# Performance work log

Measured on AMD Instinct MI355X. Metric: run time of the kernel, lower is better.

## Reference

```python
import jax, jax.numpy as jnp
import numpy as np

B, S, D, H = 4, 2048, 512, 8
DEPTH = D // H
EPS = 1e-6

def setup_inputs() -> dict:
    key = jax.random.key(0)
    ks = jax.random.split(key, 5)
    scale = 1.0 / np.sqrt(D)
    return {
        "x": jax.random.normal(ks[0], (B, S, D), dtype=jnp.float32),
        "wq": jax.random.normal(ks[1], (D, D), dtype=jnp.float32) * scale,
        "wk": jax.random.normal(ks[2], (D, D), dtype=jnp.float32) * scale,
        "wv": jax.random.normal(ks[3], (D, D), dtype=jnp.float32) * scale,
        "wo": jax.random.normal(ks[4], (D, D), dtype=jnp.float32) * scale,
        "bo": jnp.zeros((D,), dtype=jnp.float32),
        "gamma": jnp.ones((D,), dtype=jnp.float32),
        "beta": jnp.zeros((D,), dtype=jnp.float32),
    }

def _split_heads(t):
    # [B,S,D] -> [B,H,S,depth]
    return t.reshape(B, S, H, DEPTH).transpose(0, 2, 1, 3)

def reference(x, wq, wk, wv, wo, bo, gamma, beta):
    q = _split_heads(x @ wq)
    k = _split_heads(x @ wk)
    v = _split_heads(x @ wv)
    logits = jnp.einsum("bhqd,bhkd->bhqk", q, k) / jnp.sqrt(jnp.float32(DEPTH))
    attn = jax.nn.softmax(logits, axis=-1)  # dropout is identity at inference
    ctx = jnp.einsum("bhqk,bhkd->bhqd", attn, v)
    ctx = ctx.transpose(0, 2, 1, 3).reshape(B, S, D)
    out = ctx @ wo + bo
    resid = x + out  # output dropout identity at inference
    mu = jnp.mean(resid, axis=-1, keepdims=True)
    var = jnp.mean(jnp.square(resid - mu), axis=-1, keepdims=True)
    return (resid - mu) / jnp.sqrt(var + EPS) * gamma + beta
```

## Files before the change

### kernel.cpp

```cpp
#include <hip/hip_runtime.h>
#include <hip/hip_bf16.h>

typedef __attribute__((ext_vector_type(8))) short short8;
typedef __attribute__((ext_vector_type(4))) float f32x4;

constexpr int B_ = 4, S_ = 2048, D_ = 512, H_ = 8, DP_ = 64;
constexpr int M_ = B_ * S_;

__device__ __forceinline__ unsigned short f2b(float f) {
    __hip_bfloat16 h = __float2bfloat16(f);
    return *reinterpret_cast<unsigned short*>(&h);
}

__device__ __forceinline__ void gload_lds16(const unsigned short* g, unsigned short* l) {
    __builtin_amdgcn_global_load_lds((const __attribute__((address_space(1))) void*)g,
                                     (__attribute__((address_space(3))) void*)l, 16, 0, 0);
}

#define MFMA16(a, b, c) __builtin_amdgcn_mfma_f32_16x16x32_bf16((a), (b), (c), 0, 0, 0)
#define ASM_BAR() asm volatile("s_barrier" ::: "memory")

__global__ __launch_bounds__(256)
void prep(const float* __restrict__ x, unsigned short* __restrict__ xb,
          const float* __restrict__ w0, const float* __restrict__ w1,
          const float* __restrict__ w2, const float* __restrict__ w3,
          unsigned short* __restrict__ outw) {
    __shared__ float t[64][65];
    int bx = blockIdx.x;
    int tid = threadIdx.x;
    if (bx < 4096) {
        int i = bx * 256 + tid;
        float4 v = ((const float4*)x)[i];
        ushort4 o;
        o.x = f2b(v.x); o.y = f2b(v.y); o.z = f2b(v.z); o.w = f2b(v.w);
        ((ushort4*)xb)[i] = o;
        return;
    }
    int b = bx - 4096;
    int z = b >> 6, r = b & 63;
    int k0 = (r >> 3) * 64, n0 = (r & 7) * 64;
    const float* in = (z == 0) ? w0 : (z == 1) ? w1 : (z == 2) ? w2 : w3;
    unsigned short* out = outw + (size_t)z * D_ * D_;
    int tx = tid & 63, ty = tid >> 6;
#pragma unroll
    for (int i = 0; i < 16; i++) {
        int rr = ty * 16 + i;
        t[rr][tx] = in[(size_t)(k0 + rr) * D_ + n0 + tx];
    }
    __syncthreads();
#pragma unroll
    for (int i = 0; i < 16; i++) {
        int rr = ty * 16 + i;
        out[(size_t)(n0 + rr) * D_ + k0 + tx] = f2b(t[tx][rr]);
    }
}

__global__ __launch_bounds__(256, 2)
void gemm_qkvv(const unsigned short* __restrict__ X,
               const unsigned short* __restrict__ Wt,
               unsigned short* __restrict__ QKV,
               unsigned short* __restrict__ Vt) {
    int z = blockIdx.z;
    int tid = threadIdx.x;
    int wave = tid >> 6, lane = tid & 63, l16 = lane & 15, quad = lane >> 4;
    int wm = (wave >> 1) * 64, wn = (wave & 1) * 64;

    int m0, n0, bb = 0;
    const unsigned short *Abase, *Bbase;
    if (z < 2) {
        m0 = blockIdx.x * 128; n0 = blockIdx.y * 128;
        Abase = X + (size_t)m0 * D_;
        Bbase = Wt + (size_t)z * D_ * D_ + (size_t)n0 * D_;
    } else {
        int idx = blockIdx.y * 64 + blockIdx.x;
        bb = idx >> 6;
        int r = idx & 63;
        m0 = (r & 3) * 128;
        n0 = (r >> 2) * 128;
        Abase = Wt + 2 * (size_t)D_ * D_ + (size_t)m0 * D_;
        Bbase = X + ((size_t)bb * S_ + n0) * D_;
    }

    __shared__ __align__(16) unsigned short SM[32768];
    unsigned short (*Cs)[136] = reinterpret_cast<unsigned short(*)[136]>(SM);

    const int psw = l16 & 7;
    const int drow = lane >> 3;
    const int dsw = (lane & 7) ^ drow;

    auto stage = [&](int t, int b) {
        int k0 = t * 64;
        unsigned short* As = SM + b * 16384;
        unsigned short* Bs = SM + b * 16384 + 8192;
#pragma unroll
        for (int j = 0; j < 4; j++) {
            int r8 = wave * 32 + j * 8;
            gload_lds16(Abase + (size_t)(r8 + drow) * D_ + k0 + dsw * 8, As + r8 * 64);
            gload_lds16(Bbase + (size_t)(r8 + drow) * D_ + k0 + dsw * 8, Bs + r8 * 64);
        }
    };

    f32x4 acc[4][4];
    const f32x4 zf = {0.f, 0.f, 0.f, 0.f};
#pragma unroll
    for (int i = 0; i < 4; i++)
#pragma unroll
        for (int j = 0; j < 4; j++) acc[i][j] = zf;

    stage(0, 0);
    stage(1, 1);
    asm volatile("s_waitcnt vmcnt(8)" ::: "memory");
    ASM_BAR();

    for (int t = 0; t < 8; t++) {
        int b = t & 1;
        const unsigned short* As = SM + b * 16384;
        const unsigned short* Bs = SM + b * 16384 + 8192;
#pragma unroll
        for (int h = 0; h < 2; h++) {
            short8 af[4], bf[4];
#pragma unroll
            for (int mt = 0; mt < 4; mt++)
                af[mt] = *(const short8*)(As + (wm + mt * 16 + l16) * 64 + ((h * 4 + quad) ^ psw) * 8);
#pragma unroll
            for (int nt = 0; nt < 4; nt++)
                bf[nt] = *(const short8*)(Bs + (wn + nt * 16 + l16) * 64 + ((h * 4 + quad) ^ psw) * 8);
#pragma unroll
            for (int nt = 0; nt < 4; nt++)
#pragma unroll
                for (int mt = 0; mt < 4; mt++)
                    acc[nt][mt] = MFMA16(bf[nt], af[mt], acc[nt][mt]);
        }
        if (t < 7) {
            ASM_BAR();
            if (t < 6) {
                stage(t + 2, b);
                asm volatile("s_waitcnt vmcnt(8)" ::: "memory");
            } else {
                asm volatile("s_waitcnt vmcnt(0)" ::: "memory");
            }
            ASM_BAR();
        }
    }
    __syncthreads();
#pragma unroll
    for (int nt = 0; nt < 4; nt++)
#pragma unroll
        for (int mt = 0; mt < 4; mt++) {
            ushort4 pk;
            pk.x = f2b(acc[nt][mt][0]); pk.y = f2b(acc[nt][mt][1]);
            pk.z = f2b(acc[nt][mt][2]); pk.w = f2b(acc[nt][mt][3]);
            *(ushort4*)&Cs[wm + mt * 16 + l16][wn + nt * 16 + quad * 4] = pk;
        }
    __syncthreads();
    if (z < 2) {
        unsigned short* out = QKV + (size_t)z * M_ * D_;
#pragma unroll
        for (int i = 0; i < 8; i++) {
            int c = tid + i * 256;
            int ml = c >> 4, nch = c & 15;
            int m = m0 + ml, n = n0 + nch * 8;
            int b2 = m >> 11, ss = m & 2047, hh = n >> 6, dd = n & 63;
            *(short8*)(out + ((((size_t)b2 * H_ + hh) * S_ + ss) * DP_ + dd)) =
                *(const short8*)&Cs[ml][nch * 8];
        }
    } else {
#pragma unroll
        for (int i = 0; i < 8; i++) {
            int c = tid + i * 256;
            int ml = c >> 4, nch = c & 15;
            *(short8*)(Vt + ((size_t)bb * D_ + m0 + ml) * S_ + n0 + nch * 8) =
                *(const short8*)&Cs[ml][nch * 8];
        }
    }
}

__global__ __launch_bounds__(256, 3)
void flash_attn(const unsigned short* __restrict__ Qg, const unsigned short* __restrict__ Kg,
                const unsigned short* __restrict__ Vt, unsigned short* __restrict__ ctx) {
    int bid0 = blockIdx.x;
    int bid = (bid0 & 7) * 64 + (bid0 >> 3);
    int qt = bid & 15, hh = (bid >> 4) & 7, bb = bid >> 7;
    int tid = threadIdx.x;
    int wave = tid >> 6, lane = tid & 63, l16 = lane & 15, quad = lane >> 4;
    int qh = quad >> 1, ql = quad & 1;

    size_t bh = ((size_t)bb * H_ + hh) * S_ * DP_;
    const unsigned short* Qb = Qg + bh;
    const unsigned short* Kb = Kg + bh;
    const unsigned short* Vb = Vt + bh;

    __shared__ __align__(16) unsigned short Kls[2][64][64];
    __shared__ __align__(16) unsigned short Vls[2][64][64];
    __shared__ __align__(16) unsigned short Ps[4][32][64];

    const int psw = l16 & 7;
    const int drow = (lane >> 3) & 7;
    const int dsw = (lane & 7) ^ drow;

    short8 qa0, qa1, qb0, qb1;
    {
        const unsigned short* qp = Qb + (size_t)(qt * 128 + wave * 32 + l16) * DP_ + quad * 8;
        qa0 = *(const short8*)qp;
        qa1 = *(const short8*)(qp + 32);
        qb0 = *(const short8*)(qp + 16 * DP_);
        qb1 = *(const short8*)(qp + 16 * DP_ + 32);
    }

    auto stage = [&](int kv, int b) {
#pragma unroll
        for (int j = 0; j < 2; j++) {
            int r8 = (wave * 2 + j) * 8;
            int r = r8 + drow;
            gload_lds16(Kb + (size_t)(kv + r) * DP_ + dsw * 8, &Kls[b][r8][0]);
            gload_lds16(Vb + (size_t)r * S_ + kv + dsw * 8,    &Vls[b][r8][0]);
        }
    };

    stage(0, 0);
    stage(64, 1);
    asm volatile("s_waitcnt vmcnt(4)" ::: "memory");
    ASM_BAR();

    const f32x4 zf = {0.f, 0.f, 0.f, 0.f};
    f32x4 oa[4], ob[4];
#pragma unroll
    for (int i = 0; i < 4; i++) { oa[i] = zf; ob[i] = zf; }
    float m2a = -1e30f, m2b = -1e30f;
    float lsa = 0.f, lsb = 0.f;
    constexpr float c1 = 0.125f * 1.44269504088896f;

    int cur = 0;
    for (int t = 0; t < 32; t++) {
        __builtin_amdgcn_s_setprio(1);
        f32x4 sa[4], sb[4];
#pragma unroll
        for (int nt = 0; nt < 4; nt++) {
            const unsigned short* kr = &Kls[cur][nt * 16 + l16][0];
            short8 kf0 = *(const short8*)(kr + ((quad ^ psw) * 8));
            short8 kf1 = *(const short8*)(kr + (((quad ^ 4) ^ psw) * 8));
            f32x4 s = zf;
            s = MFMA16(kf0, qa0, s);
            s = MFMA16(kf1, qa1, s);
            sa[nt] = s;
            s = zf;
            s = MFMA16(kf0, qb0, s);
            s = MFMA16(kf1, qb1, s);
            sb[nt] = s;
        }
        __builtin_amdgcn_s_setprio(0);

        float ga, gb;
        {
            float ta[4], tb[4];
#pragma unroll
            for (int nt = 0; nt < 4; nt++) {
                ta[nt] = fmaxf(fmaxf(sa[nt][0], sa[nt][1]), fmaxf(sa[nt][2], sa[nt][3]));
                tb[nt] = fmaxf(fmaxf(sb[nt][0], sb[nt][1]), fmaxf(sb[nt][2], sb[nt][3]));
            }
            ga = fmaxf(fmaxf(ta[0], ta[1]), fmaxf(ta[2], ta[3]));
            gb = fmaxf(fmaxf(tb[0], tb[1]), fmaxf(tb[2], tb[3]));
        }
        ga = fmaxf(ga, __shfl_xor(ga, 16));
        ga = fmaxf(ga, __shfl_xor(ga, 32));
        gb = fmaxf(gb, __shfl_xor(gb, 16));
        gb = fmaxf(gb, __shfl_xor(gb, 32));
        ga *= c1; gb *= c1;
        float ala = 1.0f, alb = 1.0f;
        bool need = !__all((ga <= m2a + 8.0f) && (gb <= m2b + 8.0f));
        if (need) {
            float na = fmaxf(m2a, ga), nb = fmaxf(m2b, gb);
            ala = __builtin_amdgcn_exp2f(m2a - na);
            alb = __builtin_amdgcn_exp2f(m2b - nb);
            m2a = na; m2b = nb;
        }
        float rsa = 0.f, rsb = 0.f;
#pragma unroll
        for (int nt = 0; nt < 4; nt++) {
            float a0 = __builtin_amdgcn_exp2f(__builtin_fmaf(sa[nt][0], c1, -m2a));
            float a1 = __builtin_amdgcn_exp2f(__builtin_fmaf(sa[nt][1], c1, -m2a));
            float a2 = __builtin_amdgcn_exp2f(__builtin_fmaf(sa[nt][2], c1, -m2a));
            float a3 = __builtin_amdgcn_exp2f(__builtin_fmaf(sa[nt][3], c1, -m2a));
            rsa += (a0 + a1) + (a2 + a3);
            ushort4 pk;
            pk.x = f2b(a0); pk.y = f2b(a1); pk.z = f2b(a2); pk.w = f2b(a3);
            int c8 = (2 * nt + qh) ^ psw;
            *(ushort4*)&Ps[wave][l16][c8 * 8 + 4 * ql] = pk;
            float b0 = __builtin_amdgcn_exp2f(__builtin_fmaf(sb[nt][0], c1, -m2b));
            float b1 = __builtin_amdgcn_exp2f(__builtin_fmaf(sb[nt][1], c1, -m2b));
            float b2 = __builtin_amdgcn_exp2f(__builtin_fmaf(sb[nt][2], c1, -m2b));
            float b3 = __builtin_amdgcn_exp2f(__builtin_fmaf(sb[nt][3], c1, -m2b));
            rsb += (b0 + b1) + (b2 + b3);
            pk.x = f2b(b0); pk.y = f2b(b1); pk.z = f2b(b2); pk.w = f2b(b3);
            *(ushort4*)&Ps[wave][16 + l16][c8 * 8 + 4 * ql] = pk;
        }
        rsa += __shfl_xor(rsa, 16);
        rsa += __shfl_xor(rsa, 32);
        rsb += __shfl_xor(rsb, 16);
        rsb += __shfl_xor(rsb, 32);
        lsa = ala * lsa + rsa;
        lsb = alb * lsb + rsb;
        if (need) {
            float a0 = __shfl(ala, quad * 4 + 0), a1 = __shfl(ala, quad * 4 + 1);
            float a2 = __shfl(ala, quad * 4 + 2), a3 = __shfl(ala, quad * 4 + 3);
            float b0 = __shfl(alb, quad * 4 + 0), b1 = __shfl(alb, quad * 4 + 1);
            float b2 = __shfl(alb, quad * 4 + 2), b3 = __shfl(alb, quad * 4 + 3);
#pragma unroll
            for (int ot = 0; ot < 4; ot++) {
                oa[ot][0] *= a0; oa[ot][1] *= a1; oa[ot][2] *= a2; oa[ot][3] *= a3;
                ob[ot][0] *= b0; ob[ot][1] *= b1; ob[ot][2] *= b2; ob[ot][3] *= b3;
            }
        }

        __builtin_amdgcn_s_setprio(1);
#pragma unroll
        for (int kt = 0; kt < 2; kt++) {
            int pc = ((kt * 4 + quad) ^ psw) * 8;
            short8 pfA = *(const short8*)&Ps[wave][l16][pc];
            short8 pfB = *(const short8*)&Ps[wave][16 + l16][pc];
#pragma unroll
            for (int ot = 0; ot < 4; ot++) {
                short8 vf = *(const short8*)&Vls[cur][ot * 16 + l16][pc];
                oa[ot] = MFMA16(pfA, vf, oa[ot]);
                ob[ot] = MFMA16(pfB, vf, ob[ot]);
            }
        }
        __builtin_amdgcn_s_setprio(0);

        ASM_BAR();
        if (t < 30) {
            stage((t + 2) * 64, cur);
            asm volatile("s_waitcnt vmcnt(4)" ::: "memory");
        } else {
            asm volatile("s_waitcnt vmcnt(0)" ::: "memory");
        }
        ASM_BAR();
        cur ^= 1;
    }

    float la0 = __shfl(lsa, quad * 4 + 0), la1 = __shfl(lsa, quad * 4 + 1);
    float la2 = __shfl(lsa, quad * 4 + 2), la3 = __shfl(lsa, quad * 4 + 3);
    float lb0 = __shfl(lsb, quad * 4 + 0), lb1 = __shfl(lsb, quad * 4 + 1);
    float lb2 = __shfl(lsb, quad * 4 + 2), lb3 = __shfl(lsb, quad * 4 + 3);
    float ia0 = __builtin_amdgcn_rcpf(la0), ia1 = __builtin_amdgcn_rcpf(la1);
    float ia2 = __builtin_amdgcn_rcpf(la2), ia3 = __builtin_amdgcn_rcpf(la3);
    float ib0 = __builtin_amdgcn_rcpf(lb0), ib1 = __builtin_amdgcn_rcpf(lb1);
    float ib2 = __builtin_amdgcn_rcpf(lb2), ib3 = __builtin_amdgcn_rcpf(lb3);
    int srow0 = qt * 128 + wave * 32 + quad * 4;
#pragma unroll
    for (int ot = 0; ot < 4; ot++) {
        size_t base = ((size_t)bb * S_ + srow0) * D_ + hh * DP_ + ot * 16 + l16;
        ctx[base]          = f2b(oa[ot][0] * ia0);
        ctx[base + D_]     = f2b(oa[ot][1] * ia1);
        ctx[base + 2 * D_] = f2b(oa[ot][2] * ia2);
        ctx[base + 3 * D_] = f2b(oa[ot][3] * ia3);
        size_t baseB = base + (size_t)16 * D_;
        ctx[baseB]          = f2b(ob[ot][0] * ib0);
        ctx[baseB + D_]     = f2b(ob[ot][1] * ib1);
        ctx[baseB + 2 * D_] = f2b(ob[ot][2] * ib2);
        ctx[baseB + 3 * D_] = f2b(ob[ot][3] * ib3);
    }
}

__global__ __launch_bounds__(256, 2)
void gemm_proj(const unsigned short* __restrict__ A,
               const unsigned short* __restrict__ Bt,
               float* __restrict__ outf) {
    int m0 = blockIdx.x * 128, n0 = blockIdx.y * 128;
    int tid = threadIdx.x;
    int wave = tid >> 6, lane = tid & 63, l16 = lane & 15, quad = lane >> 4;
    int wm = (wave >> 1) * 64, wn = (wave & 1) * 64;

    __shared__ __align__(16) unsigned short SM[32768];

    const int psw = l16 & 7;
    const int drow = lane >> 3;
    const int dsw = (lane & 7) ^ drow;

    const unsigned short* Abase = A + (size_t)m0 * D_;
    const unsigned short* Bbase = Bt + (size_t)n0 * D_;

    auto stage = [&](int t, int b) {
        int k0 = t * 64;
        unsigned short* As = SM + b * 16384;
        unsigned short* Bs = SM + b * 16384 + 8192;
#pragma unroll
        for (int j = 0; j < 4; j++) {
            int r8 = wave * 32 + j * 8;
            gload_lds16(Abase + (size_t)(r8 + drow) * D_ + k0 + dsw * 8, As + r8 * 64);
            gload_lds16(Bbase + (size_t)(r8 + drow) * D_ + k0 + dsw * 8, Bs + r8 * 64);
        }
    };

    f32x4 acc[4][4];
    const f32x4 zf = {0.f, 0.f, 0.f, 0.f};
#pragma unroll
    for (int i = 0; i < 4; i++)
#pragma unroll
        for (int j = 0; j < 4; j++) acc[i][j] = zf;

    stage(0, 0);
    stage(1, 1);
    asm volatile("s_waitcnt vmcnt(8)" ::: "memory");
    ASM_BAR();

    for (int t = 0; t < 8; t++) {
        int b = t & 1;
        const unsigned short* As = SM + b * 16384;
        const unsigned short* Bs = SM + b * 16384 + 8192;
#pragma unroll
        for (int h = 0; h < 2; h++) {
            short8 af[4], bf[4];
#pragma unroll
            for (int mt = 0; mt < 4; mt++)
                af[mt] = *(const short8*)(As + (wm + mt * 16 + l16) * 64 + ((h * 4 + quad) ^ psw) * 8);
#pragma unroll
            for (int nt = 0; nt < 4; nt++)
                bf[nt] = *(const short8*)(Bs + (wn + nt * 16 + l16) * 64 + ((h * 4 + quad) ^ psw) * 8);
#pragma unroll
            for (int nt = 0; nt < 4; nt++)
#pragma unroll
                for (int mt = 0; mt < 4; mt++)
                    acc[nt][mt] = MFMA16(bf[nt], af[mt], acc[nt][mt]);
        }
        if (t < 7) {
            ASM_BAR();
            if (t < 6) {
                stage(t + 2, b);
                asm volatile("s_waitcnt vmcnt(8)" ::: "memory");
            } else {
                asm volatile("s_waitcnt vmcnt(0)" ::: "memory");
            }
            ASM_BAR();
        }
    }
#pragma unroll
    for (int nt = 0; nt < 4; nt++)
#pragma unroll
        for (int mt = 0; mt < 4; mt++) {
            int m = m0 + wm + mt * 16 + l16;
            int n = n0 + wn + nt * 16 + quad * 4;
            *(f32x4*)&outf[(size_t)m * D_ + n] = acc[nt][mt];
        }
}

__global__ __launch_bounds__(256, 8)
void ln_out(const float* __restrict__ tmp, const float* __restrict__ Xg,
            const float* __restrict__ bo, const float* __restrict__ gamma,
            const float* __restrict__ beta, float* __restrict__ outp) {
    int wave = threadIdx.x >> 6, lane = threadIdx.x & 63;
    int row = blockIdx.x * 4 + wave;
    const float4* t4 = (const float4*)(tmp + (size_t)row * D_);
    const float4* x4 = (const float4*)(Xg + (size_t)row * D_);
    const float4* b4 = (const float4*)bo;
    const float4* g4 = (const float4*)gamma;
    const float4* e4 = (const float4*)beta;
    float4* o4 = (float4*)(outp + (size_t)row * D_);

    float4 r[2];
    float sum = 0.f, sq = 0.f;
#pragma unroll
    for (int i = 0; i < 2; i++) {
        int c = lane + i * 64;
        float4 a = t4[c], x = x4[c], b = b4[c];
        r[i].x = a.x + x.x + b.x;
        r[i].y = a.y + x.y + b.y;
        r[i].z = a.z + x.z + b.z;
        r[i].w = a.w + x.w + b.w;
        sum += (r[i].x + r[i].y) + (r[i].z + r[i].w);
        sq += (r[i].x * r[i].x + r[i].y * r[i].y) + (r[i].z * r[i].z + r[i].w * r[i].w);
    }
#pragma unroll
    for (int off = 1; off < 64; off <<= 1) {
        sum += __shfl_xor(sum, off);
        sq += __shfl_xor(sq, off);
    }
    float mu = sum * (1.0f / D_);
    float var = sq * (1.0f / D_) - mu * mu;
    float rstd = rsqrtf(var + 1e-6f);
#pragma unroll
    for (int i = 0; i < 2; i++) {
        int c = lane + i * 64;
        float4 g = g4[c], e = e4[c];
        float4 o;
        o.x = (r[i].x - mu) * rstd * g.x + e.x;
        o.y = (r[i].y - mu) * rstd * g.y + e.y;
        o.z = (r[i].z - mu) * rstd * g.z + e.z;
        o.w = (r[i].w - mu) * rstd * g.w + e.w;
        o4[c] = o;
    }
}

extern "C" void kernel_launch(void* const* d_in, const int* in_sizes, int n_in,
                              void* d_out, int out_size, void* d_ws, size_t ws_size,
                              hipStream_t stream) {
    const float* x     = (const float*)d_in[0];
    const float* wq    = (const float*)d_in[1];
    const float* wk    = (const float*)d_in[2];
    const float* wv    = (const float*)d_in[3];
    const float* wo    = (const float*)d_in[4];
    const float* bo    = (const float*)d_in[5];
    const float* gamma = (const float*)d_in[6];
    const float* beta  = (const float*)d_in[7];
    float* out = (float*)d_out;

    unsigned short* xb  = (unsigned short*)d_ws;
    unsigned short* wt  = xb + (size_t)M_ * D_;
    unsigned short* Q   = wt + 4 * D_ * D_;
    unsigned short* K   = Q + (size_t)M_ * D_;
    unsigned short* Vt  = K + (size_t)M_ * D_;
    unsigned short* ctx = xb;
    float* tmp = (float*)Q;

    prep<<<dim3(4096 + 256), 256, 0, stream>>>(x, xb, wq, wk, wv, wo, wt);
    gemm_qkvv<<<dim3(64, 4, 3), 256, 0, stream>>>(xb, wt, Q, Vt);
    flash_attn<<<dim3(512), 256, 0, stream>>>(Q, K, Vt, ctx);
    gemm_proj<<<dim3(64, 4), 256, 0, stream>>>(ctx, wt + 3 * (size_t)D_ * D_, tmp);
    ln_out<<<dim3(2048), 256, 0, stream>>>(tmp, x, bo, gamma, beta, out);
}
```

Before: 178.2 us.

## Widen flash-attention KV tile to 128 and split PV into two halves

```diff
diff --git a/kernel.cpp b/kernel.cpp
--- a/kernel.cpp
+++ b/kernel.cpp
@@ -175,7 +175,7 @@
     }
 }
 
-__global__ __launch_bounds__(256, 3)
+__global__ __launch_bounds__(256, 2)
 void flash_attn(const unsigned short* __restrict__ Qg, const unsigned short* __restrict__ Kg,
                 const unsigned short* __restrict__ Vt, unsigned short* __restrict__ ctx) {
     int bid0 = blockIdx.x;
@@ -190,13 +190,14 @@
     const unsigned short* Kb = Kg + bh;
     const unsigned short* Vb = Vt + bh;
 
-    __shared__ __align__(16) unsigned short Kls[2][64][64];
-    __shared__ __align__(16) unsigned short Vls[2][64][64];
+    __shared__ __align__(16) unsigned short Kls[2][128][64];
+    __shared__ __align__(16) unsigned short Vls[2][64][128];
     __shared__ __align__(16) unsigned short Ps[4][32][64];
 
     const int psw = l16 & 7;
-    const int drow = (lane >> 3) & 7;
-    const int dsw = (lane & 7) ^ drow;
+    const int drowK = (lane >> 3) & 7;
+    const int lcK = (lane & 7) ^ drowK;
+    const int dvo = lane >> 4;
 
     short8 qa0, qa1, qb0, qb1;
     {
@@ -209,17 +210,22 @@
 
     auto stage = [&](int kv, int b) {
 #pragma unroll
-        for (int j = 0; j < 2; j++) {
-            int r8 = (wave * 2 + j) * 8;
-            int r = r8 + drow;
-            gload_lds16(Kb + (size_t)(kv + r) * DP_ + dsw * 8, &Kls[b][r8][0]);
-            gload_lds16(Vb + (size_t)r * S_ + kv + dsw * 8,    &Vls[b][r8][0]);
+        for (int j = 0; j < 4; j++) {
+            int r8 = (wave * 4 + j) * 8;
+            gload_lds16(Kb + (size_t)(kv + r8 + drowK) * DP_ + lcK * 8, &Kls[b][r8][0]);
+        }
+#pragma unroll
+        for (int j = 0; j < 4; j++) {
+            int r4 = (wave * 4 + j) * 4;
+            int dv = r4 + dvo;
+            int lcV = (lane & 15) ^ (dv & 7);
+            gload_lds16(Vb + (size_t)dv * S_ + kv + lcV * 8, &Vls[b][r4][0]);
         }
     };
 
     stage(0, 0);
-    stage(64, 1);
-    asm volatile("s_waitcnt vmcnt(4)" ::: "memory");
+    stage(128, 1);
+    asm volatile("s_waitcnt vmcnt(8)" ::: "memory");
     ASM_BAR();
 
     const f32x4 zf = {0.f, 0.f, 0.f, 0.f};
@@ -231,11 +237,11 @@
     constexpr float c1 = 0.125f * 1.44269504088896f;
 
     int cur = 0;
-    for (int t = 0; t < 32; t++) {
+    for (int t = 0; t < 16; t++) {
         __builtin_amdgcn_s_setprio(1);
-        f32x4 sa[4], sb[4];
-#pragma unroll
-        for (int nt = 0; nt < 4; nt++) {
+        f32x4 sa[8], sb[8];
+#pragma unroll
+        for (int nt = 0; nt < 8; nt++) {
             const unsigned short* kr = &Kls[cur][nt * 16 + l16][0];
             short8 kf0 = *(const short8*)(kr + ((quad ^ psw) * 8));
             short8 kf1 = *(const short8*)(kr + (((quad ^ 4) ^ psw) * 8));
@@ -252,14 +258,16 @@
 
         float ga, gb;
         {
-            float ta[4], tb[4];
-#pragma unroll
-            for (int nt = 0; nt < 4; nt++) {
+            float ta[8], tb[8];
+#pragma unroll
+            for (int nt = 0; nt < 8; nt++) {
                 ta[nt] = fmaxf(fmaxf(sa[nt][0], sa[nt][1]), fmaxf(sa[nt][2], sa[nt][3]));
                 tb[nt] = fmaxf(fmaxf(sb[nt][0], sb[nt][1]), fmaxf(sb[nt][2], sb[nt][3]));
             }
-            ga = fmaxf(fmaxf(ta[0], ta[1]), fmaxf(ta[2], ta[3]));
-            gb = fmaxf(fmaxf(tb[0], tb[1]), fmaxf(tb[2], tb[3]));
+            ga = fmaxf(fmaxf(fmaxf(ta[0], ta[1]), fmaxf(ta[2], ta[3])),
+                       fmaxf(fmaxf(ta[4], ta[5]), fmaxf(ta[6], ta[7])));
+            gb = fmaxf(fmaxf(fmaxf(tb[0], tb[1]), fmaxf(tb[2], tb[3])),
+                       fmaxf(fmaxf(tb[4], tb[5]), fmaxf(tb[6], tb[7])));
         }
         ga = fmaxf(ga, __shfl_xor(ga, 16));
         ga = fmaxf(ga, __shfl_xor(ga, 32));
@@ -274,25 +282,55 @@
             alb = __builtin_amdgcn_exp2f(m2b - nb);
             m2a = na; m2b = nb;
         }
+        if (need) {
+            float a0 = __shfl(ala, quad * 4 + 0), a1 = __shfl(ala, quad * 4 + 1);
+            float a2 = __shfl(ala, quad * 4 + 2), a3 = __shfl(ala, quad * 4 + 3);
+            float b0 = __shfl(alb, quad * 4 + 0), b1 = __shfl(alb, quad * 4 + 1);
+            float b2 = __shfl(alb, quad * 4 + 2), b3 = __shfl(alb, quad * 4 + 3);
+#pragma unroll
+            for (int ot = 0; ot < 4; ot++) {
+                oa[ot][0] *= a0; oa[ot][1] *= a1; oa[ot][2] *= a2; oa[ot][3] *= a3;
+                ob[ot][0] *= b0; ob[ot][1] *= b1; ob[ot][2] *= b2; ob[ot][3] *= b3;
+            }
+        }
+
         float rsa = 0.f, rsb = 0.f;
 #pragma unroll
-        for (int nt = 0; nt < 4; nt++) {
-            float a0 = __builtin_amdgcn_exp2f(__builtin_fmaf(sa[nt][0], c1, -m2a));
-            float a1 = __builtin_amdgcn_exp2f(__builtin_fmaf(sa[nt][1], c1, -m2a));
-            float a2 = __builtin_amdgcn_exp2f(__builtin_fmaf(sa[nt][2], c1, -m2a));
-            float a3 = __builtin_amdgcn_exp2f(__builtin_fmaf(sa[nt][3], c1, -m2a));
-            rsa += (a0 + a1) + (a2 + a3);
-            ushort4 pk;
-            pk.x = f2b(a0); pk.y = f2b(a1); pk.z = f2b(a2); pk.w = f2b(a3);
-            int c8 = (2 * nt + qh) ^ psw;
-            *(ushort4*)&Ps[wave][l16][c8 * 8 + 4 * ql] = pk;
-            float b0 = __builtin_amdgcn_exp2f(__builtin_fmaf(sb[nt][0], c1, -m2b));
-            float b1 = __builtin_amdgcn_exp2f(__builtin_fmaf(sb[nt][1], c1, -m2b));
-            float b2 = __builtin_amdgcn_exp2f(__builtin_fmaf(sb[nt][2], c1, -m2b));
-            float b3 = __builtin_amdgcn_exp2f(__builtin_fmaf(sb[nt][3], c1, -m2b));
-            rsb += (b0 + b1) + (b2 + b3);
-            pk.x = f2b(b0); pk.y = f2b(b1); pk.z = f2b(b2); pk.w = f2b(b3);
-            *(ushort4*)&Ps[wave][16 + l16][c8 * 8 + 4 * ql] = pk;
+        for (int h = 0; h < 2; h++) {
+#pragma unroll
+            for (int ntl = 0; ntl < 4; ntl++) {
+                int nt = h * 4 + ntl;
+                float a0 = __builtin_amdgcn_exp2f(__builtin_fmaf(sa[nt][0], c1, -m2a));
+                float a1 = __builtin_amdgcn_exp2f(__builtin_fmaf(sa[nt][1], c1, -m2a));
+                float a2 = __builtin_amdgcn_exp2f(__builtin_fmaf(sa[nt][2], c1, -m2a));
+                float a3 = __builtin_amdgcn_exp2f(__builtin_fmaf(sa[nt][3], c1, -m2a));
+                rsa += (a0 + a1) + (a2 + a3);
+                ushort4 pk;
+                pk.x = f2b(a0); pk.y = f2b(a1); pk.z = f2b(a2); pk.w = f2b(a3);
+                int c8 = (2 * ntl + qh) ^ psw;
+                *(ushort4*)&Ps[wave][l16][c8 * 8 + 4 * ql] = pk;
+                float b0 = __builtin_amdgcn_exp2f(__builtin_fmaf(sb[nt][0], c1, -m2b));
+                float b1 = __builtin_amdgcn_exp2f(__builtin_fmaf(sb[nt][1], c1, -m2b));
+                float b2 = __builtin_amdgcn_exp2f(__builtin_fmaf(sb[nt][2], c1, -m2b));
+                float b3 = __builtin_amdgcn_exp2f(__builtin_fmaf(sb[nt][3], c1, -m2b));
+                rsb += (b0 + b1) + (b2 + b3);
+                pk.x = f2b(b0); pk.y = f2b(b1); pk.z = f2b(b2); pk.w = f2b(b3);
+                *(ushort4*)&Ps[wave][16 + l16][c8 * 8 + 4 * ql] = pk;
+            }
+            __builtin_amdgcn_s_setprio(1);
+#pragma unroll
+            for (int kt = 0; kt < 2; kt++) {
+                int pcl = (kt * 4 + quad) ^ psw;
+                short8 pfA = *(const short8*)&Ps[wave][l16][pcl * 8];
+                short8 pfB = *(const short8*)&Ps[wave][16 + l16][pcl * 8];
+#pragma unroll
+                for (int ot = 0; ot < 4; ot++) {
+                    short8 vf = *(const short8*)&Vls[cur][ot * 16 + l16][(h * 8 + pcl) * 8];
+                    oa[ot] = MFMA16(pfA, vf, oa[ot]);
+                    ob[ot] = MFMA16(pfB, vf, ob[ot]);
+                }
+            }
+            __builtin_amdgcn_s_setprio(0);
         }
         rsa += __shfl_xor(rsa, 16);
         rsa += __shfl_xor(rsa, 32);
@@ -300,41 +338,17 @@
         rsb += __shfl_xor(rsb, 32);
         lsa = ala * lsa + rsa;
         lsb = alb * lsb + rsb;
-        if (need) {
-            float a0 = __shfl(ala, quad * 4 + 0), a1 = __shfl(ala, quad * 4 + 1);
-            float a2 = __shfl(ala, quad * 4 + 2), a3 = __shfl(ala, quad * 4 + 3);
-            float b0 = __shfl(alb, quad * 4 + 0), b1 = __shfl(alb, quad * 4 + 1);
-            float b2 = __shfl(alb, quad * 4 + 2), b3 = __shfl(alb, quad * 4 + 3);
-#pragma unroll
-            for (int ot = 0; ot < 4; ot++) {
-                oa[ot][0] *= a0; oa[ot][1] *= a1; oa[ot][2] *= a2; oa[ot][3] *= a3;
-                ob[ot][0] *= b0; ob[ot][1] *= b1; ob[ot][2] *= b2; ob[ot][3] *= b3;
-            }
-        }
-
-        __builtin_amdgcn_s_setprio(1);
-#pragma unroll
-        for (int kt = 0; kt < 2; kt++) {
-            int pc = ((kt * 4 + quad) ^ psw) * 8;
-            short8 pfA = *(const short8*)&Ps[wave][l16][pc];
-            short8 pfB = *(const short8*)&Ps[wave][16 + l16][pc];
-#pragma unroll
-            for (int ot = 0; ot < 4; ot++) {
-                short8 vf = *(const short8*)&Vls[cur][ot * 16 + l16][pc];
-                oa[ot] = MFMA16(pfA, vf, oa[ot]);
-                ob[ot] = MFMA16(pfB, vf, ob[ot]);
-            }
-        }
-        __builtin_amdgcn_s_setprio(0);
-
-        ASM_BAR();
-        if (t < 30) {
-            stage((t + 2) * 64, cur);
-            asm volatile("s_waitcnt vmcnt(4)" ::: "memory");
-        } else {
-            asm volatile("s_waitcnt vmcnt(0)" ::: "memory");
-        }
-        ASM_BAR();
+
+        if (t < 15) {
+            ASM_BAR();
+            if (t < 14) {
+                stage((t + 2) * 128, cur);
+                asm volatile("s_waitcnt vmcnt(8)" ::: "memory");
+            } else {
+                asm volatile("s_waitcnt vmcnt(0)" ::: "memory");
+            }
+            ASM_BAR();
+        }
         cur ^= 1;
     }
 
```

Result: no change. 174.9 us (-1.8%).
